# Optimization experiments

Hardware: AMD Instinct MI355X
Metric: run time of the kernel (lower is better)

The kernel has to match this reference:

```python
import jax, jax.numpy as jnp
import numpy as np

N = 65536
HID = 768
NH = 12
HD = HID // NH  # 64


def setup_inputs() -> dict:
    key = jax.random.key(0)
    ks = jax.random.split(key, 9)
    s = 1.0 / np.sqrt(HID)
    return {
        "x": jax.random.normal(ks[0], (N, HID), jnp.float32),
        "Wq": jax.random.normal(ks[1], (HID, HID), jnp.float32) * s,
        "bq": jax.random.normal(ks[2], (HID,), jnp.float32) * s,
        "Wk": jax.random.normal(ks[3], (HID, HID), jnp.float32) * s,
        "bk": jax.random.normal(ks[4], (HID,), jnp.float32) * s,
        "Wv": jax.random.normal(ks[5], (HID, HID), jnp.float32) * s,
        "bv": jax.random.normal(ks[6], (HID,), jnp.float32) * s,
        "Wo": jax.random.normal(ks[7], (HID, HID), jnp.float32) * s,
        "bo": jax.random.normal(ks[8], (HID,), jnp.float32) * s,
    }


def reference(x, Wq, bq, Wk, bk, Wv, bv, Wo, bo):
    # torch.nn.Linear: y = x @ W.T + b
    Q = x @ Wq.T + bq                       # [N, HID]
    K = x @ Wk.T + bk
    V = x @ Wv.T + bv
    Qh = Q.reshape(N, NH, HD)               # [N, H, D]
    Kh = K.reshape(N, HD, NH)               # [N, D, H]  (faithful to source's view)
    Vh = V.reshape(N, NH, HD)               # [N, H, D]
    # per-token head-vs-head scores: [N, H, H]
    scores = jnp.einsum('nhd,ndg->nhg', Qh, Kh) / np.sqrt(HD).astype(np.float32)
    attn = jax.nn.softmax(scores, axis=-1)  # dropout is identity in eval mode
    ctx = jnp.einsum('nhg,ngd->nhd', attn, Vh).reshape(N, HID)
    return ctx @ Wo.T + bo
```

## Files before the change

### kernel.cpp

```cpp
#include <hip/hip_runtime.h>
#include <hip/hip_bf16.h>
#include <cstdint>
#include <cstddef>

#define N_TOK 65536
#define HIDDEN 768
#define NHEAD 12
#define HEADD 64

typedef __bf16 bf16x8 __attribute__((ext_vector_type(8)));
typedef float f32x4 __attribute__((ext_vector_type(4)));

__device__ __forceinline__ float bflo(unsigned int u) {
  return __builtin_bit_cast(float, (unsigned int)(u << 16));
}
__device__ __forceinline__ float bfhi(unsigned int u) {
  return __builtin_bit_cast(float, (unsigned int)(u & 0xffff0000u));
}
__device__ __forceinline__ unsigned short f2bf(float f) {
  unsigned int x = __builtin_bit_cast(unsigned int, f);
  unsigned int r = x + 0x7fffu + ((x >> 16) & 1u);
  return (unsigned short)(r >> 16);
}

__device__ __forceinline__ void gload_lds16(const void* g, void* l) {
  __builtin_amdgcn_global_load_lds(
      (const __attribute__((address_space(1))) void*)g,
      (__attribute__((address_space(3))) void*)l, 16, 0, 0);
}

__device__ __forceinline__ bf16x8 ldsfrag(const char* base, int row, int kb) {
  int L = (row << 7) + kb;
  L ^= (row & 7) << 4;
  return *(const bf16x8*)(base + L);
}

__device__ __forceinline__ int swz(int loff) {
  return loff ^ (((loff >> 7) & 7) << 4);
}

__global__ void cvt_all_kernel(const float* __restrict__ x,
                               const float* __restrict__ Wq, const float* __restrict__ Wk,
                               const float* __restrict__ Wv, const float* __restrict__ Wo,
                               const float* __restrict__ bq, const float* __restrict__ bk,
                               const float* __restrict__ bv,
                               unsigned short* __restrict__ x_bf,
                               unsigned short* __restrict__ wqkv,
                               unsigned short* __restrict__ wo_bf,
                               float* __restrict__ bqkv) {
  const int bid = blockIdx.x;
  if (bid < 49152) {
    const int idx = bid * 256 + threadIdx.x;
    float4 v = ((const float4*)x)[idx];
    ushort4 o;
    o.x = f2bf(v.x); o.y = f2bf(v.y); o.z = f2bf(v.z); o.w = f2bf(v.w);
    ((ushort4*)x_bf)[idx] = o;
  } else if (bid < 51456) {
    const int wb = bid - 49152;
    const int mat = wb / 576;
    const int idx = (wb - mat * 576) * 256 + threadIdx.x;
    const float* src = mat == 0 ? Wq : mat == 1 ? Wk : mat == 2 ? Wv : Wo;
    unsigned short* dst = (mat == 3) ? wo_bf : wqkv + mat * (HIDDEN * HIDDEN);
    float4 v = ((const float4*)src)[idx];
    ushort4 o;
    o.x = f2bf(v.x); o.y = f2bf(v.y); o.z = f2bf(v.z); o.w = f2bf(v.w);
    ((ushort4*)dst)[idx] = o;
  } else {
    const int i = (bid - 51456) * 256 + threadIdx.x;
    if (i < 576) {
      const float* src = i < 192 ? bq : i < 384 ? bk : bv;
      const int off = i < 192 ? i : i < 384 ? i - 192 : i - 384;
      ((float4*)bqkv)[i] = ((const float4*)src)[off];
    }
  }
}

template <int MODE>
__global__ __launch_bounds__(512, 2)
void gemm256(const unsigned short* __restrict__ A,
             const unsigned short* __restrict__ B,
             const float* __restrict__ bias,
             void* __restrict__ C, int K, int NBLK, int ldc) {
  __shared__ __align__(16) char lds[131072];
  const int tid = threadIdx.x;
  const int lane = tid & 63;
  const int wave = tid >> 6;
  const int wr = wave >> 2;
  const int wc = wave & 3;

  const int nwg = gridDim.x;
  const int bid = blockIdx.x;
  const int wg = (bid & 7) * (nwg >> 3) + (bid >> 3);
  const int mb = wg / NBLK;
  const int nb = wg - mb * NBLK;
  const int brow = mb << 8;
  const int bcol = nb << 8;

  const int Ld = tid * 16;
  const int Ls = Ld ^ (((tid >> 3) & 7) << 4);
  const int sr = Ls >> 7;
  const int sc = (Ls & 127) >> 1;

  const int NT = K >> 6;

#define STAGE(Mat, panelRow, bufbase, matoff, half, kt)                         \
  do {                                                                          \
    const unsigned short* _s =                                                  \
        (Mat) + (size_t)((panelRow) + (half) * 128 + sr) * K + ((kt) << 6) + sc;\
    char* _d = (char*)lds + (bufbase) + (matoff) + ((half) << 14) + Ld;         \
    gload_lds16(_s, _d);                                                        \
    gload_lds16(_s + ((size_t)K << 6), _d + 8192);                              \
  } while (0)

  f32x4 acc[8][4];
#pragma unroll
  for (int m = 0; m < 8; ++m)
#pragma unroll
    for (int n = 0; n < 4; ++n) acc[m][n] = (f32x4){0.f, 0.f, 0.f, 0.f};

  const int arow = wr * 128 + (lane & 15);
  const int nrow = wc * 64 + (lane & 15);
  const int kpart = (lane >> 4) * 16;

  STAGE(A, brow, 0, 0, 0, 0);
  STAGE(A, brow, 0, 0, 1, 0);
  STAGE(B, bcol, 0, 32768, 0, 0);
  STAGE(B, bcol, 0, 32768, 1, 0);
  asm volatile("s_waitcnt vmcnt(0)" ::: "memory");
  __builtin_amdgcn_s_barrier();

  for (int t = 0; t < NT; ++t) {
    const int cur = t & 1;
    const char* la = lds + cur * 65536;
    const char* lb = la + 32768;
    const int obuf = (cur ^ 1) * 65536;

    bf16x8 aLo[8], aHi[8], bLo[4], bHi[4];

#pragma unroll
    for (int m = 0; m < 4; ++m)
#pragma unroll
      for (int kk = 0; kk < 2; ++kk)
        aLo[m * 2 + kk] = ldsfrag(la, arow + m * 16, kk * 64 + kpart);
#pragma unroll
    for (int n = 0; n < 2; ++n)
#pragma unroll
      for (int kk = 0; kk < 2; ++kk)
        bLo[n * 2 + kk] = ldsfrag(lb, nrow + n * 16, kk * 64 + kpart);
    if (t + 1 < NT) {
      STAGE(A, brow, obuf, 0, 0, t + 1);
      STAGE(A, brow, obuf, 0, 1, t + 1);
    }
    __builtin_amdgcn_s_barrier();
    asm volatile("s_waitcnt lgkmcnt(0)" ::: "memory");
    __builtin_amdgcn_s_setprio(1);
#pragma unroll
    for (int m = 0; m < 4; ++m)
#pragma unroll
      for (int n = 0; n < 2; ++n)
#pragma unroll
        for (int kk = 0; kk < 2; ++kk)
          acc[m][n] = __builtin_amdgcn_mfma_f32_16x16x32_bf16(
              aLo[m * 2 + kk], bLo[n * 2 + kk], acc[m][n], 0, 0, 0);
    __builtin_amdgcn_s_setprio(0);

#pragma unroll
    for (int m = 0; m < 4; ++m)
#pragma unroll
      for (int kk = 0; kk < 2; ++kk)
        aHi[m * 2 + kk] = ldsfrag(la, arow + 64 + m * 16, kk * 64 + kpart);
    if (t + 1 < NT) {
      STAGE(B, bcol, obuf, 32768, 0, t + 1);
      STAGE(B, bcol, obuf, 32768, 1, t + 1);
    }
    __builtin_amdgcn_s_barrier();
    asm volatile("s_waitcnt lgkmcnt(0)" ::: "memory");
    __builtin_amdgcn_s_setprio(1);
#pragma unroll
    for (int m = 0; m < 4; ++m)
#pragma unroll
      for (int n = 0; n < 2; ++n)
#pragma unroll
        for (int kk = 0; kk < 2; ++kk)
          acc[4 + m][n] = __builtin_amdgcn_mfma_f32_16x16x32_bf16(
              aHi[m * 2 + kk], bLo[n * 2 + kk], acc[4 + m][n], 0, 0, 0);
    __builtin_amdgcn_s_setprio(0);

#pragma unroll
    for (int n = 0; n < 2; ++n)
#pragma unroll
      for (int kk = 0; kk < 2; ++kk)
        bHi[n * 2 + kk] = ldsfrag(lb, nrow + 32 + n * 16, kk * 64 + kpart);
    __builtin_amdgcn_s_barrier();
    asm volatile("s_waitcnt lgkmcnt(0)" ::: "memory");
    __builtin_amdgcn_s_setprio(1);
#pragma unroll
    for (int m = 0; m < 4; ++m)
#pragma unroll
      for (int n = 0; n < 2; ++n)
#pragma unroll
        for (int kk = 0; kk < 2; ++kk)
          acc[4 + m][n + 2] = __builtin_amdgcn_mfma_f32_16x16x32_bf16(
              aHi[m * 2 + kk], bHi[n * 2 + kk], acc[4 + m][n + 2], 0, 0, 0);
    __builtin_amdgcn_s_setprio(0);

    asm volatile("s_waitcnt vmcnt(0)" ::: "memory");
    __builtin_amdgcn_s_barrier();
    __builtin_amdgcn_s_setprio(1);
#pragma unroll
    for (int m = 0; m < 4; ++m)
#pragma unroll
      for (int n = 0; n < 2; ++n)
#pragma unroll
        for (int kk = 0; kk < 2; ++kk)
          acc[m][n + 2] = __builtin_amdgcn_mfma_f32_16x16x32_bf16(
              aLo[m * 2 + kk], bHi[n * 2 + kk], acc[m][n + 2], 0, 0, 0);
    __builtin_amdgcn_s_setprio(0);
  }
#undef STAGE

  const int crow0 = brow + wr * 128 + (lane >> 4) * 4;
  const int ccol0 = bcol + wc * 64 + (lane & 15);
#pragma unroll
  for (int m = 0; m < 8; ++m) {
#pragma unroll
    for (int n = 0; n < 4; ++n) {
      const int col = ccol0 + n * 16;
      const float bv = bias[col];
#pragma unroll
      for (int r = 0; r < 4; ++r) {
        const int row = crow0 + m * 16 + r;
        const float v = acc[m][n][r] + bv;
        if (MODE == 1)
          ((float*)C)[(size_t)row * ldc + col] = v;
        else
          ((unsigned short*)C)[(size_t)row * ldc + col] = f2bf(v);
      }
    }
  }
}

#define T_BLK 16
#define ROWB 4624

__global__ __launch_bounds__(256)
void attn_kernel(const unsigned short* __restrict__ qkv,
                 unsigned short* __restrict__ ctx) {
  __shared__ __align__(16) char lds[T_BLK * ROWB];
  const int tid = threadIdx.x;
  const int blk = blockIdx.x;

  const uint4* src = (const uint4*)(qkv + (size_t)blk * (T_BLK * 2304));
#pragma unroll
  for (int it = 0; it < 18; ++it) {
    const int l = it * 256 + tid;
    const uint4 v = src[l];
    const int tok = l / 288;
    const int loff = (l - tok * 288) * 16;
    *(uint4*)(lds + tok * ROWB + swz(loff)) = v;
  }
  __syncthreads();

  if (tid < 192) {
    const int tok = tid / 12;
    const int h = tid - tok * 12;
    const char* rowb = lds + tok * ROWB;

    float s[12];
#pragma unroll
    for (int g = 0; g < 12; ++g) s[g] = 0.f;
#pragma unroll
    for (int c = 0; c < 8; ++c) {
      const uint4 qc = *(const uint4*)(rowb + swz(h * 128 + c * 16));
      const unsigned int qw[4] = {qc.x, qc.y, qc.z, qc.w};
      float qd[8];
#pragma unroll
      for (int w = 0; w < 4; ++w) {
        qd[2 * w] = bflo(qw[w]);
        qd[2 * w + 1] = bfhi(qw[w]);
      }
#pragma unroll
      for (int j = 0; j < 8; ++j) {
        const int koff = 1536 + (c * 8 + j) * 24;
        const uint2 k0 = *(const uint2*)(rowb + swz(koff));
        const uint2 k1 = *(const uint2*)(rowb + swz(koff + 8));
        const uint2 k2 = *(const uint2*)(rowb + swz(koff + 16));
        const float q = qd[j];
        s[0] += q * bflo(k0.x);  s[1] += q * bfhi(k0.x);
        s[2] += q * bflo(k0.y);  s[3] += q * bfhi(k0.y);
        s[4] += q * bflo(k1.x);  s[5] += q * bfhi(k1.x);
        s[6] += q * bflo(k1.y);  s[7] += q * bfhi(k1.y);
        s[8] += q * bflo(k2.x);  s[9] += q * bfhi(k2.x);
        s[10] += q * bflo(k2.y); s[11] += q * bfhi(k2.y);
      }
    }

    float mx = s[0];
#pragma unroll
    for (int g = 1; g < 12; ++g) mx = fmaxf(mx, s[g]);
    float p[12];
    float sum = 0.f;
#pragma unroll
    for (int g = 0; g < 12; ++g) {
      p[g] = __expf((s[g] - mx) * 0.125f);
      sum += p[g];
    }
    const float inv = 1.0f / sum;
#pragma unroll
    for (int g = 0; g < 12; ++g) p[g] *= inv;

    unsigned short* op = ctx + ((size_t)(blk * T_BLK + tok)) * 768 + h * 64;
#pragma unroll
    for (int c = 0; c < 8; ++c) {
      float o[8];
#pragma unroll
      for (int k = 0; k < 8; ++k) o[k] = 0.f;
#pragma unroll
      for (int g = 0; g < 12; ++g) {
        const uint4 vv = *(const uint4*)(rowb + swz(3072 + g * 128 + c * 16));
        const unsigned int vw[4] = {vv.x, vv.y, vv.z, vv.w};
#pragma unroll
        for (int k = 0; k < 4; ++k) {
          o[2 * k] += p[g] * bflo(vw[k]);
          o[2 * k + 1] += p[g] * bfhi(vw[k]);
        }
      }
      uint4 w;
      w.x = (unsigned int)f2bf(o[0]) | ((unsigned int)f2bf(o[1]) << 16);
      w.y = (unsigned int)f2bf(o[2]) | ((unsigned int)f2bf(o[3]) << 16);
      w.z = (unsigned int)f2bf(o[4]) | ((unsigned int)f2bf(o[5]) << 16);
      w.w = (unsigned int)f2bf(o[6]) | ((unsigned int)f2bf(o[7]) << 16);
      *(uint4*)(op + c * 8) = w;
    }
  }
}

extern "C" void kernel_launch(void* const* d_in, const int* in_sizes, int n_in,
                              void* d_out, int out_size, void* d_ws, size_t ws_size,
                              hipStream_t stream) {
  const float* x = (const float*)d_in[0];
  const float* Wq = (const float*)d_in[1];
  const float* bq = (const float*)d_in[2];
  const float* Wk = (const float*)d_in[3];
  const float* bk = (const float*)d_in[4];
  const float* Wv = (const float*)d_in[5];
  const float* bv = (const float*)d_in[6];
  const float* Wo = (const float*)d_in[7];
  const float* bo = (const float*)d_in[8];
  float* out = (float*)d_out;

  char* ws = (char*)d_ws;
  unsigned short* x_bf = (unsigned short*)ws;
  unsigned short* ctx = (unsigned short*)ws;
  unsigned short* qkv = (unsigned short*)(ws + 100663296u);
  unsigned short* wqkv = (unsigned short*)(ws + 402653184u);
  unsigned short* wo_bf = (unsigned short*)(ws + 406192128u);
  float* bqkv = (float*)(ws + 407371776u);

  cvt_all_kernel<<<51459, 256, 0, stream>>>(x, Wq, Wk, Wv, Wo, bq, bk, bv,
                                            x_bf, wqkv, wo_bf, bqkv);

  gemm256<0><<<(N_TOK / 256) * (2304 / 256), 512, 0, stream>>>(
      x_bf, wqkv, bqkv, qkv, HIDDEN, 2304 / 256, 2304);

  attn_kernel<<<N_TOK / T_BLK, 256, 0, stream>>>(qkv, ctx);

  gemm256<1><<<(N_TOK / 256) * (HIDDEN / 256), 512, 0, stream>>>(
      ctx, wo_bf, bo, out, HIDDEN, HIDDEN / 256, HIDDEN);
}
```

Baseline: 523.4 us.

## Use 16 waves per 256x256 GEMM tile with smaller per-wave accumulators

The GEMM workgroup grows from 512 to 1024 threads, so each wave owns a 64x64 output sub-tile instead of 128x64, which halves the accumulator and fragment registers per wave. Each thread now issues one global-to-LDS load per stage instead of two, and the K loop is re-phased into four half-K steps with sched_barriers pinning the MFMA clusters. The goal is more waves in flight to hide LDS and global latency. The cost is more barriers per wave, a lower MFMA-to-LDS-read ratio per wave, and only one 128KB-LDS workgroup per CU.

New measurement: 518.3 us. About the same (-1.0%).

```diff
diff --git a/kernel.cpp b/kernel.cpp
--- a/kernel.cpp
+++ b/kernel.cpp
@@ -76,7 +76,7 @@
 }
 
 template <int MODE>
-__global__ __launch_bounds__(512, 2)
+__global__ __launch_bounds__(1024)
 void gemm256(const unsigned short* __restrict__ A,
              const unsigned short* __restrict__ B,
              const float* __restrict__ bias,
@@ -109,16 +109,15 @@
         (Mat) + (size_t)((panelRow) + (half) * 128 + sr) * K + ((kt) << 6) + sc;\
     char* _d = (char*)lds + (bufbase) + (matoff) + ((half) << 14) + Ld;         \
     gload_lds16(_s, _d);                                                        \
-    gload_lds16(_s + ((size_t)K << 6), _d + 8192);                              \
   } while (0)
 
-  f32x4 acc[8][4];
-#pragma unroll
-  for (int m = 0; m < 8; ++m)
+  f32x4 acc[4][4];
+#pragma unroll
+  for (int m = 0; m < 4; ++m)
 #pragma unroll
     for (int n = 0; n < 4; ++n) acc[m][n] = (f32x4){0.f, 0.f, 0.f, 0.f};
 
-  const int arow = wr * 128 + (lane & 15);
+  const int arow = wr * 64 + (lane & 15);
   const int nrow = wc * 64 + (lane & 15);
   const int kpart = (lane >> 4) * 16;
 
@@ -134,95 +133,82 @@
     const char* la = lds + cur * 65536;
     const char* lb = la + 32768;
     const int obuf = (cur ^ 1) * 65536;
-
-    bf16x8 aLo[8], aHi[8], bLo[4], bHi[4];
-
-#pragma unroll
-    for (int m = 0; m < 4; ++m)
-#pragma unroll
-      for (int kk = 0; kk < 2; ++kk)
-        aLo[m * 2 + kk] = ldsfrag(la, arow + m * 16, kk * 64 + kpart);
-#pragma unroll
-    for (int n = 0; n < 2; ++n)
-#pragma unroll
-      for (int kk = 0; kk < 2; ++kk)
-        bLo[n * 2 + kk] = ldsfrag(lb, nrow + n * 16, kk * 64 + kpart);
-    if (t + 1 < NT) {
-      STAGE(A, brow, obuf, 0, 0, t + 1);
-      STAGE(A, brow, obuf, 0, 1, t + 1);
-    }
+    const bool pf = (t + 1 < NT);
+
+    bf16x8 aF[4], bLo[2], bHi[2];
+
+#pragma unroll
+    for (int m = 0; m < 4; ++m) aF[m] = ldsfrag(la, arow + m * 16, kpart);
+#pragma unroll
+    for (int n = 0; n < 2; ++n) bLo[n] = ldsfrag(lb, nrow + n * 16, kpart);
+    if (pf) STAGE(A, brow, obuf, 0, 0, t + 1);
     __builtin_amdgcn_s_barrier();
     asm volatile("s_waitcnt lgkmcnt(0)" ::: "memory");
+    __builtin_amdgcn_sched_barrier(0);
     __builtin_amdgcn_s_setprio(1);
 #pragma unroll
     for (int m = 0; m < 4; ++m)
 #pragma unroll
       for (int n = 0; n < 2; ++n)
-#pragma unroll
-        for (int kk = 0; kk < 2; ++kk)
-          acc[m][n] = __builtin_amdgcn_mfma_f32_16x16x32_bf16(
-              aLo[m * 2 + kk], bLo[n * 2 + kk], acc[m][n], 0, 0, 0);
+        acc[m][n] = __builtin_amdgcn_mfma_f32_16x16x32_bf16(aF[m], bLo[n],
+                                                            acc[m][n], 0, 0, 0);
     __builtin_amdgcn_s_setprio(0);
 
 #pragma unroll
-    for (int m = 0; m < 4; ++m)
-#pragma unroll
-      for (int kk = 0; kk < 2; ++kk)
-        aHi[m * 2 + kk] = ldsfrag(la, arow + 64 + m * 16, kk * 64 + kpart);
-    if (t + 1 < NT) {
-      STAGE(B, bcol, obuf, 32768, 0, t + 1);
-      STAGE(B, bcol, obuf, 32768, 1, t + 1);
-    }
+    for (int n = 0; n < 2; ++n) bHi[n] = ldsfrag(lb, nrow + 32 + n * 16, kpart);
+    if (pf) STAGE(A, brow, obuf, 0, 1, t + 1);
     __builtin_amdgcn_s_barrier();
     asm volatile("s_waitcnt lgkmcnt(0)" ::: "memory");
+    __builtin_amdgcn_sched_barrier(0);
     __builtin_amdgcn_s_setprio(1);
 #pragma unroll
     for (int m = 0; m < 4; ++m)
 #pragma unroll
       for (int n = 0; n < 2; ++n)
-#pragma unroll
-        for (int kk = 0; kk < 2; ++kk)
-          acc[4 + m][n] = __builtin_amdgcn_mfma_f32_16x16x32_bf16(
-              aHi[m * 2 + kk], bLo[n * 2 + kk], acc[4 + m][n], 0, 0, 0);
+        acc[m][n + 2] = __builtin_amdgcn_mfma_f32_16x16x32_bf16(
+            aF[m], bHi[n], acc[m][n + 2], 0, 0, 0);
     __builtin_amdgcn_s_setprio(0);
 
 #pragma unroll
-    for (int n = 0; n < 2; ++n)
-#pragma unroll
-      for (int kk = 0; kk < 2; ++kk)
-        bHi[n * 2 + kk] = ldsfrag(lb, nrow + 32 + n * 16, kk * 64 + kpart);
+    for (int m = 0; m < 4; ++m) aF[m] = ldsfrag(la, arow + m * 16, 64 + kpart);
+#pragma unroll
+    for (int n = 0; n < 2; ++n) bLo[n] = ldsfrag(lb, nrow + n * 16, 64 + kpart);
+    if (pf) STAGE(B, bcol, obuf, 32768, 0, t + 1);
     __builtin_amdgcn_s_barrier();
     asm volatile("s_waitcnt lgkmcnt(0)" ::: "memory");
+    __builtin_amdgcn_sched_barrier(0);
     __builtin_amdgcn_s_setprio(1);
 #pragma unroll
     for (int m = 0; m < 4; ++m)
 #pragma unroll
       for (int n = 0; n < 2; ++n)
-#pragma unroll
-        for (int kk = 0; kk < 2; ++kk)
-          acc[4 + m][n + 2] = __builtin_amdgcn_mfma_f32_16x16x32_bf16(
-              aHi[m * 2 + kk], bHi[n * 2 + kk], acc[4 + m][n + 2], 0, 0, 0);
+        acc[m][n] = __builtin_amdgcn_mfma_f32_16x16x32_bf16(aF[m], bLo[n],
+                                                            acc[m][n], 0, 0, 0);
     __builtin_amdgcn_s_setprio(0);
 
+#pragma unroll
+    for (int n = 0; n < 2; ++n)
+      bHi[n] = ldsfrag(lb, nrow + 32 + n * 16, 64 + kpart);
+    if (pf) STAGE(B, bcol, obuf, 32768, 1, t + 1);
     asm volatile("s_waitcnt vmcnt(0)" ::: "memory");
     __builtin_amdgcn_s_barrier();
+    asm volatile("s_waitcnt lgkmcnt(0)" ::: "memory");
+    __builtin_amdgcn_sched_barrier(0);
     __builtin_amdgcn_s_setprio(1);
 #pragma unroll
     for (int m = 0; m < 4; ++m)
 #pragma unroll
       for (int n = 0; n < 2; ++n)
-#pragma unroll
-        for (int kk = 0; kk < 2; ++kk)
-          acc[m][n + 2] = __builtin_amdgcn_mfma_f32_16x16x32_bf16(
-              aLo[m * 2 + kk], bHi[n * 2 + kk], acc[m][n + 2], 0, 0, 0);
+        acc[m][n + 2] = __builtin_amdgcn_mfma_f32_16x16x32_bf16(
+            aF[m], bHi[n], acc[m][n + 2], 0, 0, 0);
     __builtin_amdgcn_s_setprio(0);
   }
 #undef STAGE
 
-  const int crow0 = brow + wr * 128 + (lane >> 4) * 4;
+  const int crow0 = brow + wr * 64 + (lane >> 4) * 4;
   const int ccol0 = bcol + wc * 64 + (lane & 15);
 #pragma unroll
-  for (int m = 0; m < 8; ++m) {
+  for (int m = 0; m < 4; ++m) {
 #pragma unroll
     for (int n = 0; n < 4; ++n) {
       const int col = ccol0 + n * 16;
@@ -360,11 +346,11 @@
   cvt_all_kernel<<<51459, 256, 0, stream>>>(x, Wq, Wk, Wv, Wo, bq, bk, bv,
                                             x_bf, wqkv, wo_bf, bqkv);
 
-  gemm256<0><<<(N_TOK / 256) * (2304 / 256), 512, 0, stream>>>(
+  gemm256<0><<<(N_TOK / 256) * (2304 / 256), 1024, 0, stream>>>(
       x_bf, wqkv, bqkv, qkv, HIDDEN, 2304 / 256, 2304);
 
   attn_kernel<<<N_TOK / T_BLK, 256, 0, stream>>>(qkv, ctx);
 
-  gemm256<1><<<(N_TOK / 256) * (HIDDEN / 256), 512, 0, stream>>>(
+  gemm256<1><<<(N_TOK / 256) * (HIDDEN / 256), 1024, 0, stream>>>(
       ctx, wo_bf, bo, out, HIDDEN, HIDDEN / 256, HIDDEN);
 }
```
